# Kernel tuning notes

Hardware: AMD Instinct MI355X
Metric: run time of the kernel (lower is better)

The kernel has to match this reference:

```python
import jax, jax.numpy as jnp
import numpy as np


def _disk_samples(size):
    # Same construction as the torch module: regular grid on [-1,1]^2, keep points in unit disk.
    xs, ys = [], []
    for i in range(size):
        for j in range(size):
            x = i * 2.0 / (size - 1) - 1.0
            y = j * 2.0 / (size - 1) - 1.0
            if x * x + y * y <= 1.0:
                xs.append(x)
                ys.append(y)
    return np.asarray(xs, np.float32), np.asarray(ys, np.float32)


def setup_inputs() -> dict:
    key = jax.random.key(0)
    k1, k2, k3, k4, k5 = jax.random.split(key, 5)
    B, L, C, H, W = 1, 12, 3, 640, 640
    images = jax.random.uniform(k1, (B, L, C, H, W), dtype=jnp.float32)
    alphas = jax.random.uniform(k2, (B, L, 1, H, W), dtype=jnp.float32)
    coffs = jax.random.uniform(k3, (B, L, 1, H, W), dtype=jnp.float32)  # per-plane disparity-like map in [0,1)
    K = jax.random.uniform(k4, (B, 1, 1, 1), dtype=jnp.float32) * 20.0 + 2.0  # aperture radius in pixels
    depth_focus = jax.random.uniform(k5, (B, 1, 1, 1), dtype=jnp.float32)  # focus value, same units as coffs
    return {"images": images, "alphas": alphas, "coffs": coffs, "K": K,
            "depth_focus": depth_focus, "samples_per_side": 5}


def reference(images, alphas, coffs, K, depth_focus, samples_per_side):
    # Depth-aware ray-traced bokeh over an MPI stack.
    # For each output pixel and each circular aperture sample (u,v), gather from each
    # plane at an offset proportional to the plane's signed defocus radius
    #   r = K * (coff - depth_focus)
    # (nearest-pixel gather, clamped), then composite planes front-to-back with alpha,
    # and average over aperture samples.
    B, L, C, H, W = images.shape
    xs_np, ys_np = _disk_samples(int(samples_per_side))
    n_samples = len(xs_np)

    Kb = K[:, 0, 0, 0]                      # [B]
    df = depth_focus[:, 0, 0, 0]            # [B]
    coff = coffs[:, :, 0]                   # [B,L,H,W]
    r = Kb[:, None, None, None] * (coff - df[:, None, None, None])  # signed radius per plane/pixel

    a_flat = alphas[:, :, 0].reshape(B, L, H * W)       # [B,L,HW]
    img_flat = images.reshape(B, L, C, H * W)           # [B,L,C,HW]
    yy, xx = jnp.meshgrid(jnp.arange(H, dtype=jnp.float32),
                          jnp.arange(W, dtype=jnp.float32), indexing="ij")

    acc = jnp.zeros((B, C, H, W), images.dtype)
    for s in range(n_samples):  # small fixed aperture-sample set (static)
        qx = jnp.clip(jnp.round(xx + xs_np[s] * r), 0, W - 1).astype(jnp.int32)
        qy = jnp.clip(jnp.round(yy + ys_np[s] * r), 0, H - 1).astype(jnp.int32)
        idx = (qy * W + qx).reshape(B, L, H * W)
        a = jnp.take_along_axis(a_flat, idx, axis=2)                 # [B,L,HW]
        c = jnp.take_along_axis(img_flat, idx[:, :, None, :], axis=3)  # [B,L,C,HW]
        trans = jnp.cumprod(1.0 - a, axis=1)
        excl = jnp.concatenate([jnp.ones_like(a[:, :1]), trans[:, :-1]], axis=1)
        w = a * excl                                                  # front-to-back weights
        acc = acc + (w[:, :, None, :] * c).sum(axis=1).reshape(B, C, H, W)
    return acc / jnp.float32(n_samples)
```

## Files before the change

kernel.cpp:

```cpp
#include <hip/hip_runtime.h>

#define L_ 12
#define H_ 640
#define W_ 640
#define HW_ (H_*W_)

#define TS 40
#define HALO 22
#define LD (TS + 2*HALO)
#define NSLOT (LD*LD)
#define NT 1024
#define SIZE 5
#define NSAMP 13

__global__ __launch_bounds__(NT, 4) void render_tiled(
    const float* __restrict__ images,
    const float* __restrict__ alphas,
    const float* __restrict__ coffs,
    const float* __restrict__ Kp,
    const float* __restrict__ dfp,
    float* __restrict__ out) {
  __shared__ float4 tile[NSLOT];

  const int tid = threadIdx.x;
  const int tx0 = (int)(blockIdx.x % (W_ / TS)) * TS;
  const int ty0 = (int)(blockIdx.x / (W_ / TS)) * TS;
  const int bx0 = tx0 - HALO;
  const int by0 = ty0 - HALO;

  const float Kv = Kp[0];
  const float df = dfp[0];

  const bool has2 = (tid < TS * TS - NT);
  const int p1 = tid + NT;

  const int x0 = tx0 + (tid % TS), y0 = ty0 + (tid / TS);
  const int x1 = tx0 + (p1 % TS), y1 = ty0 + (p1 / TS);
  const float xf0 = (float)x0, yf0 = (float)y0;
  const float xf1 = (float)x1, yf1 = (float)y1;
  const int rowbase0 = (y0 - by0) * LD, colbase0 = x0 - bx0;
  const int rowbase1 = (y1 - by0) * LD, colbase1 = x1 - bx0;
  const int src0 = y0 * W_ + x0;
  const int src1 = y1 * W_ + x1;

  float T0[NSAMP], T1[NSAMP];
#pragma unroll
  for (int s = 0; s < NSAMP; ++s) { T0[s] = 1.f; T1[s] = 1.f; }
  float a00 = 0.f, a01 = 0.f, a02 = 0.f;
  float a10 = 0.f, a11 = 0.f, a12 = 0.f;

  for (int l = 0; l < L_; ++l) {
    __syncthreads();
    const float* __restrict__ aP  = alphas + (size_t)l * HW_;
    const float* __restrict__ c0P = images + (size_t)(l * 3 + 0) * HW_;
    const float* __restrict__ c1P = images + (size_t)(l * 3 + 1) * HW_;
    const float* __restrict__ c2P = images + (size_t)(l * 3 + 2) * HW_;
    for (int s = tid; s < NSLOT; s += NT) {
      int hy = s / LD, hx = s - hy * LD;
      int gy = min(max(by0 + hy, 0), H_ - 1);
      int gx = min(max(bx0 + hx, 0), W_ - 1);
      int g = gy * W_ + gx;
      tile[s] = make_float4(aP[g], c0P[g], c1P[g], c2P[g]);
    }
    __syncthreads();

    const float r0 = __fmul_rn(Kv, __fsub_rn(coffs[(size_t)l * HW_ + src0], df));
    const float r1 = has2 ? __fmul_rn(Kv, __fsub_rn(coffs[(size_t)l * HW_ + src1], df)) : 0.f;

    int ord = 0;
#pragma unroll
    for (int i = 0; i < SIZE; ++i) {
#pragma unroll
      for (int j = 0; j < SIZE; ++j) {
        const double dx = (double)i * 2.0 / (SIZE - 1) - 1.0;
        const double dy = (double)j * 2.0 / (SIZE - 1) - 1.0;
        if (dx * dx + dy * dy <= 1.0) {
          const float sx = (float)dx;
          const float sy = (float)dy;
          {
            int cx, ro;
            if (dx == 0.0) {
              cx = colbase0;
            } else {
              float qxf = rintf(__fadd_rn(xf0, __fmul_rn(sx, r0)));
              qxf = fminf(fmaxf(qxf, 0.f), (float)(W_ - 1));
              cx = (int)qxf - bx0;
            }
            if (dy == 0.0) {
              ro = rowbase0;
            } else {
              float qyf = rintf(__fadd_rn(yf0, __fmul_rn(sy, r0)));
              qyf = fminf(fmaxf(qyf, 0.f), (float)(H_ - 1));
              ro = ((int)qyf - by0) * LD;
            }
            float4 v = tile[ro + cx];
            float w = v.x * T0[ord];
            a00 = __fmaf_rn(w, v.y, a00);
            a01 = __fmaf_rn(w, v.z, a01);
            a02 = __fmaf_rn(w, v.w, a02);
            T0[ord] *= (1.f - v.x);
          }
          if (has2) {
            int cx, ro;
            if (dx == 0.0) {
              cx = colbase1;
            } else {
              float qxf = rintf(__fadd_rn(xf1, __fmul_rn(sx, r1)));
              qxf = fminf(fmaxf(qxf, 0.f), (float)(W_ - 1));
              cx = (int)qxf - bx0;
            }
            if (dy == 0.0) {
              ro = rowbase1;
            } else {
              float qyf = rintf(__fadd_rn(yf1, __fmul_rn(sy, r1)));
              qyf = fminf(fmaxf(qyf, 0.f), (float)(H_ - 1));
              ro = ((int)qyf - by0) * LD;
            }
            float4 v = tile[ro + cx];
            float w = v.x * T1[ord];
            a10 = __fmaf_rn(w, v.y, a10);
            a11 = __fmaf_rn(w, v.z, a11);
            a12 = __fmaf_rn(w, v.w, a12);
            T1[ord] *= (1.f - v.x);
          }
          ++ord;
        }
      }
    }
  }

  const float n = (float)NSAMP;
  out[0 * HW_ + src0] = a00 / n;
  out[1 * HW_ + src0] = a01 / n;
  out[2 * HW_ + src0] = a02 / n;
  if (has2) {
    out[0 * HW_ + src1] = a10 / n;
    out[1 * HW_ + src1] = a11 / n;
    out[2 * HW_ + src1] = a12 / n;
  }
}

extern "C" void kernel_launch(void* const* d_in, const int* in_sizes, int n_in,
                              void* d_out, int out_size, void* d_ws, size_t ws_size,
                              hipStream_t stream) {
  const float* images = (const float*)d_in[0];
  const float* alphas = (const float*)d_in[1];
  const float* coffs  = (const float*)d_in[2];
  const float* Kp     = (const float*)d_in[3];
  const float* dfp    = (const float*)d_in[4];
  float* out = (float*)d_out;

  const int tiles = (W_ / TS) * (H_ / TS);
  render_tiled<<<dim3(tiles), dim3(NT), 0, stream>>>(
      images, alphas, coffs, Kp, dfp, out);
}
```

Baseline: 175.4 us.

## Shrink tiles, load only the radius-bounded halo, and swizzle block order

Reduces the output tile from 40x40 to 20x20 with 512 threads (one pixel per thread) and pads the shared tile to a 64-wide row so indexing uses shifts. It computes the maximum defocus radius from K and depth_focus at runtime and loads only the halo rows that radius can reach. It also swizzles the block index to change the tile scheduling order. The intent is to cut global loads of unused halo rows and raise occupancy, but smaller tiles raise the halo-to-interior ratio, column halo is still loaded at full width, and 112 of 512 threads sit idle during compute.

```diff
diff --git a/kernel.cpp b/kernel.cpp
--- a/kernel.cpp
+++ b/kernel.cpp
@@ -5,11 +5,12 @@
 #define W_ 640
 #define HW_ (H_*W_)
 
-#define TS 40
+#define TS 20
 #define HALO 22
-#define LD (TS + 2*HALO)
+#define LD 64
 #define NSLOT (LD*LD)
-#define NT 1024
+#define NT 512
+#define NPX (TS*TS)
 #define SIZE 5
 #define NSAMP 13
 
@@ -23,31 +24,33 @@
   __shared__ float4 tile[NSLOT];
 
   const int tid = threadIdx.x;
-  const int tx0 = (int)(blockIdx.x % (W_ / TS)) * TS;
-  const int ty0 = (int)(blockIdx.x / (W_ / TS)) * TS;
+  const int nwg = (W_ / TS) * (H_ / TS);
+  const int bid = (int)blockIdx.x;
+  const int swz = (bid & 7) * (nwg >> 3) + (bid >> 3);
+  const int tx0 = (swz % (W_ / TS)) * TS;
+  const int ty0 = (swz / (W_ / TS)) * TS;
   const int bx0 = tx0 - HALO;
   const int by0 = ty0 - HALO;
 
   const float Kv = Kp[0];
   const float df = dfp[0];
 
-  const bool has2 = (tid < TS * TS - NT);
-  const int p1 = tid + NT;
+  int Hrt = (int)ceilf(__fmul_rn(Kv, fmaxf(df, 1.f - df))) + 1;
+  Hrt = min(Hrt, HALO);
+  const int hy0 = HALO - Hrt;
+  const int nslots = (TS + 2 * Hrt) << 6;
+  const int rowoff = hy0 << 6;
 
+  const bool haspx = (tid < NPX);
   const int x0 = tx0 + (tid % TS), y0 = ty0 + (tid / TS);
-  const int x1 = tx0 + (p1 % TS), y1 = ty0 + (p1 / TS);
   const float xf0 = (float)x0, yf0 = (float)y0;
-  const float xf1 = (float)x1, yf1 = (float)y1;
-  const int rowbase0 = (y0 - by0) * LD, colbase0 = x0 - bx0;
-  const int rowbase1 = (y1 - by0) * LD, colbase1 = x1 - bx0;
+  const int rowbase0 = (y0 - by0) << 6, colbase0 = x0 - bx0;
   const int src0 = y0 * W_ + x0;
-  const int src1 = y1 * W_ + x1;
 
-  float T0[NSAMP], T1[NSAMP];
+  float T0[NSAMP];
 #pragma unroll
-  for (int s = 0; s < NSAMP; ++s) { T0[s] = 1.f; T1[s] = 1.f; }
+  for (int s = 0; s < NSAMP; ++s) T0[s] = 1.f;
   float a00 = 0.f, a01 = 0.f, a02 = 0.f;
-  float a10 = 0.f, a11 = 0.f, a12 = 0.f;
 
   for (int l = 0; l < L_; ++l) {
     __syncthreads();
@@ -55,29 +58,29 @@
     const float* __restrict__ c0P = images + (size_t)(l * 3 + 0) * HW_;
     const float* __restrict__ c1P = images + (size_t)(l * 3 + 1) * HW_;
     const float* __restrict__ c2P = images + (size_t)(l * 3 + 2) * HW_;
-    for (int s = tid; s < NSLOT; s += NT) {
-      int hy = s / LD, hx = s - hy * LD;
+    for (int s = tid; s < nslots; s += NT) {
+      int hy = (s >> 6) + hy0;
+      int hx = s & 63;
       int gy = min(max(by0 + hy, 0), H_ - 1);
       int gx = min(max(bx0 + hx, 0), W_ - 1);
       int g = gy * W_ + gx;
-      tile[s] = make_float4(aP[g], c0P[g], c1P[g], c2P[g]);
+      tile[s + rowoff] = make_float4(aP[g], c0P[g], c1P[g], c2P[g]);
     }
     __syncthreads();
 
-    const float r0 = __fmul_rn(Kv, __fsub_rn(coffs[(size_t)l * HW_ + src0], df));
-    const float r1 = has2 ? __fmul_rn(Kv, __fsub_rn(coffs[(size_t)l * HW_ + src1], df)) : 0.f;
+    if (haspx) {
+      const float r0 = __fmul_rn(Kv, __fsub_rn(coffs[(size_t)l * HW_ + src0], df));
 
-    int ord = 0;
+      int ord = 0;
 #pragma unroll
-    for (int i = 0; i < SIZE; ++i) {
+      for (int i = 0; i < SIZE; ++i) {
 #pragma unroll
-      for (int j = 0; j < SIZE; ++j) {
-        const double dx = (double)i * 2.0 / (SIZE - 1) - 1.0;
-        const double dy = (double)j * 2.0 / (SIZE - 1) - 1.0;
-        if (dx * dx + dy * dy <= 1.0) {
-          const float sx = (float)dx;
-          const float sy = (float)dy;
-          {
+        for (int j = 0; j < SIZE; ++j) {
+          const double dx = (double)i * 2.0 / (SIZE - 1) - 1.0;
+          const double dy = (double)j * 2.0 / (SIZE - 1) - 1.0;
+          if (dx * dx + dy * dy <= 1.0) {
+            const float sx = (float)dx;
+            const float sy = (float)dy;
             int cx, ro;
             if (dx == 0.0) {
               cx = colbase0;
@@ -91,7 +94,7 @@
             } else {
               float qyf = rintf(__fadd_rn(yf0, __fmul_rn(sy, r0)));
               qyf = fminf(fmaxf(qyf, 0.f), (float)(H_ - 1));
-              ro = ((int)qyf - by0) * LD;
+              ro = ((int)qyf - by0) << 6;
             }
             float4 v = tile[ro + cx];
             float w = v.x * T0[ord];
@@ -99,44 +102,18 @@
             a01 = __fmaf_rn(w, v.z, a01);
             a02 = __fmaf_rn(w, v.w, a02);
             T0[ord] *= (1.f - v.x);
+            ++ord;
           }
-          if (has2) {
-            int cx, ro;
-            if (dx == 0.0) {
-              cx = colbase1;
-            } else {
-              float qxf = rintf(__fadd_rn(xf1, __fmul_rn(sx, r1)));
-              qxf = fminf(fmaxf(qxf, 0.f), (float)(W_ - 1));
-              cx = (int)qxf - bx0;
-            }
-            if (dy == 0.0) {
-              ro = rowbase1;
-            } else {
-              float qyf = rintf(__fadd_rn(yf1, __fmul_rn(sy, r1)));
-              qyf = fminf(fmaxf(qyf, 0.f), (float)(H_ - 1));
-              ro = ((int)qyf - by0) * LD;
-            }
-            float4 v = tile[ro + cx];
-            float w = v.x * T1[ord];
-            a10 = __fmaf_rn(w, v.y, a10);
-            a11 = __fmaf_rn(w, v.z, a11);
-            a12 = __fmaf_rn(w, v.w, a12);
-            T1[ord] *= (1.f - v.x);
-          }
-          ++ord;
         }
       }
     }
   }
 
-  const float n = (float)NSAMP;
-  out[0 * HW_ + src0] = a00 / n;
-  out[1 * HW_ + src0] = a01 / n;
-  out[2 * HW_ + src0] = a02 / n;
-  if (has2) {
-    out[0 * HW_ + src1] = a10 / n;
-    out[1 * HW_ + src1] = a11 / n;
-    out[2 * HW_ + src1] = a12 / n;
+  if (haspx) {
+    const float n = (float)NSAMP;
+    out[0 * HW_ + src0] = a00 / n;
+    out[1 * HW_ + src0] = a01 / n;
+    out[2 * HW_ + src0] = a02 / n;
   }
 }
 
```

Result: slower. 189.0 us (+7.7%).
